# Kernel optimization log

Hardware: AMD Instinct MI355X
Metric: run time of the kernel (lower is better)

The kernel has to match this reference:

```python
import jax, jax.numpy as jnp
import numpy as np

B, S, E, H, P, F = 8, 512, 512, 8, 64, 2048
D = E // H  # head_dim = 64
EPS = 1e-5


def layernorm(x, g, b):
    mu = jnp.mean(x, axis=-1, keepdims=True)
    var = jnp.mean((x - mu) ** 2, axis=-1, keepdims=True)
    return (x - mu) * jax.lax.rsqrt(var + EPS) * g + b


def setup_inputs() -> dict:
    key = jax.random.key(0)
    ks = jax.random.split(key, 20)
    s = 1.0 / np.sqrt(E)
    inp = {
        "x": jax.random.normal(ks[0], (B, S, E), jnp.float32),
        "dist": jax.random.uniform(ks[1], (B, S, S), jnp.float32),
        "delatimes": jax.random.randint(ks[2], (B, S), 0, 128, jnp.int32),
        "mask": jnp.ones((B, S), jnp.int32),
        "wq_w": jax.random.uniform(ks[3], (E, E), jnp.float32, -s, s),
        "wq_b": jnp.zeros((E,), jnp.float32),
        "wk_w": jax.random.uniform(ks[4], (E, E), jnp.float32, -s, s),
        "wk_b": jnp.zeros((E,), jnp.float32),
        "wv_w": jax.random.uniform(ks[5], (E, E), jnp.float32, -s, s),
        "wv_b": jnp.zeros((E,), jnp.float32),
        "wo_w": jax.random.uniform(ks[6], (E, E), jnp.float32, -s, s),
        "wo_b": jnp.zeros((E,), jnp.float32),
        "pos_emb": jax.random.normal(ks[7], (2 * P + 1, D), jnp.float32),
        "w1": jax.random.uniform(ks[8], (E, F), jnp.float32, -s, s),
        "b1": jnp.zeros((F,), jnp.float32),
        "w2": jax.random.uniform(ks[9], (F, E), jnp.float32, -1.0 / np.sqrt(F), 1.0 / np.sqrt(F)),
        "b2": jnp.zeros((E,), jnp.float32),
        "ln1_g": jnp.ones((E,), jnp.float32),
        "ln1_b": jnp.zeros((E,), jnp.float32),
        "ln2_g": jnp.ones((E,), jnp.float32),
        "ln2_b": jnp.zeros((E,), jnp.float32),
    }
    return inp


def reference(x, dist, delatimes, mask, wq_w, wq_b, wk_w, wk_b, wv_w, wv_b,
              wo_w, wo_b, pos_emb, w1, b1, w2, b2, ln1_g, ln1_b, ln2_g, ln2_b):
    # relative-time embedding indices [B,S,S]
    rel = delatimes[:, None, :] - delatimes[:, :, None]
    idx = jnp.clip(rel, -P, P) + P
    z = pos_emb[idx]  # [B,S,S,D]

    def heads(t, w, b):
        return (t @ w + b).reshape(B, S, H, D).transpose(0, 2, 1, 3)  # [B,H,S,D]

    q = heads(x, wq_w, wq_b)
    k = heads(x, wk_w, wk_b)
    v = heads(x, wv_w, wv_b)

    scale = D ** -0.5
    scores = jnp.einsum('bhid,bhjd->bhij', q, k) + jnp.einsum('bhid,bijd->bhij', q, z)
    w = scores * scale + 0.6 * dist[:, None, :, :]
    pad = mask[:, None, None, :]  # [B,1,1,S]
    w = jnp.where(pad == 0, -1e9, w)
    aw = jax.nn.softmax(w, axis=-1)

    attn = jnp.einsum('bhij,bhjd->bhid', aw, v) + jnp.einsum('bhij,bijd->bhid', aw, z)
    concat = attn.transpose(0, 2, 1, 3).reshape(B, S, E)
    attn_out = layernorm(x + (concat @ wo_w + wo_b), ln1_g, ln1_b)

    ffn = jax.nn.relu(attn_out @ w1 + b1) @ w2 + b2
    return layernorm(attn_out + ffn, ln2_g, ln2_b)
```

## Files before the change

### kernel.cpp

```cpp
#include <hip/hip_runtime.h>
#include <hip/hip_bf16.h>

typedef __bf16 bf16x8 __attribute__((ext_vector_type(8)));
typedef float f32x4 __attribute__((ext_vector_type(4)));

#define TOKENS 4096
#define EDIM 512
#define FDIM 2048
#define SEQ 512
#define NHEAD 8
#define HDIM 64
#define QKVS 1536

__global__ __launch_bounds__(256) void prep(
    const float* __restrict__ wq_w, const float* __restrict__ wk_w,
    const float* __restrict__ wv_w, const float* __restrict__ wo_w,
    const float* __restrict__ w1, const float* __restrict__ w2,
    const float* __restrict__ x, const float* __restrict__ dist,
    const float* __restrict__ wq_b, const float* __restrict__ wk_b,
    const float* __restrict__ wv_b,
    __bf16* __restrict__ wqkvt, __bf16* __restrict__ wot,
    __bf16* __restrict__ w1t, __bf16* __restrict__ w2t,
    __bf16* __restrict__ xb, __bf16* __restrict__ distb,
    float* __restrict__ qkvb) {
  __shared__ float t[32][33];
  int bid = blockIdx.x;
  if (bid < 3072) {
    const float* src;
    __bf16* dst;
    int R = 512, C = 512, bx, by;
    if (bid < 1024) {
      int seg = bid >> 8, local = bid & 255;
      src = seg == 0 ? wq_w : seg == 1 ? wk_w : seg == 2 ? wv_w : wo_w;
      dst = seg == 0 ? wqkvt : seg == 1 ? wqkvt + 262144 : seg == 2 ? wqkvt + 524288 : wot;
      bx = local & 15; by = local >> 4;
    } else if (bid < 2048) {
      int local = bid - 1024; src = w1; dst = w1t; C = 2048;
      bx = local & 63; by = local >> 6;
    } else {
      int local = bid - 2048; src = w2; dst = w2t; R = 2048;
      bx = local & 15; by = local >> 4;
    }
    int c0 = bx * 32, r0 = by * 32;
    int tx = threadIdx.x & 31, ty = threadIdx.x >> 5;
    for (int rr = ty; rr < 32; rr += 8)
      t[rr][tx] = src[(size_t)(r0 + rr) * C + c0 + tx];
    __syncthreads();
    for (int rr = ty; rr < 32; rr += 8)
      dst[(size_t)(c0 + rr) * R + r0 + tx] = (__bf16)t[tx][rr];
  } else if (bid < 4096) {
    int i = (bid - 3072) * 256 + threadIdx.x;
    float4 a = ((const float4*)x)[i * 2];
    float4 b4 = ((const float4*)x)[i * 2 + 1];
    bf16x8 p;
    p[0] = (__bf16)a.x; p[1] = (__bf16)a.y; p[2] = (__bf16)a.z; p[3] = (__bf16)a.w;
    p[4] = (__bf16)b4.x; p[5] = (__bf16)b4.y; p[6] = (__bf16)b4.z; p[7] = (__bf16)b4.w;
    ((bf16x8*)xb)[i] = p;
  } else if (bid == 4096) {
    for (int i = threadIdx.x; i < 1536; i += 256)
      qkvb[i] = i < 512 ? wq_b[i] : i < 1024 ? wk_b[i - 512] : wv_b[i - 1024];
  } else {
    int i = (bid - 4097) * 256 + threadIdx.x;
    float4 a = ((const float4*)dist)[i * 2];
    float4 b4 = ((const float4*)dist)[i * 2 + 1];
    bf16x8 p;
    p[0] = (__bf16)a.x; p[1] = (__bf16)a.y; p[2] = (__bf16)a.z; p[3] = (__bf16)a.w;
    p[4] = (__bf16)b4.x; p[5] = (__bf16)b4.y; p[6] = (__bf16)b4.z; p[7] = (__bf16)b4.w;
    ((bf16x8*)distb)[i] = p;
  }
}

__device__ __forceinline__ void gl_lds16(const void* g, void* l) {
  __builtin_amdgcn_global_load_lds(
      (const __attribute__((address_space(1))) unsigned int*)(size_t)g,
      (__attribute__((address_space(3))) unsigned int*)(size_t)l, 16, 0, 0);
}

template <int BN>
__global__ __launch_bounds__(256) void gemm128(
    const __bf16* __restrict__ A, const __bf16* __restrict__ Bt,
    const float* __restrict__ bias, const float* __restrict__ resid,
    float* __restrict__ Cf, __bf16* __restrict__ Cb,
    int M, int N, int K, int relu) {
  constexpr int NI = BN / 32;
  __shared__ __attribute__((aligned(16))) __bf16 Asl[128 * 64];
  __shared__ __attribute__((aligned(16))) __bf16 Bsl[BN * 64];
  const int tid = threadIdx.x, w = tid >> 6, lane = tid & 63;
  const int c = lane & 15, g = lane >> 4;
  const int m0 = blockIdx.y * 128, n0 = blockIdx.x * BN;
  const int wr = w >> 1, wc = w & 1;
  f32x4 acc[4][NI] = {};
  const __bf16* Ab = A + (size_t)m0 * K;
  const __bf16* Bb = Bt + (size_t)n0 * K;

  for (int k0 = 0; k0 < K; k0 += 64) {
#pragma unroll
    for (int s = 0; s < 4; s++) {
      int L = (s * 256 + tid) * 16;
      int row = L >> 7;
      int lslot = ((L >> 4) & 7) ^ (row & 7);
      gl_lds16(Ab + (size_t)row * K + k0 + lslot * 8,
               (char*)Asl + s * 4096 + w * 1024);
    }
#pragma unroll
    for (int s = 0; s < NI; s++) {
      int L = (s * 256 + tid) * 16;
      int row = L >> 7;
      int lslot = ((L >> 4) & 7) ^ (row & 7);
      gl_lds16(Bb + (size_t)row * K + k0 + lslot * 8,
               (char*)Bsl + s * 4096 + w * 1024);
    }
    __syncthreads();

    bf16x8 af[4][2], bfr[NI][2];
#pragma unroll
    for (int mi = 0; mi < 4; mi++)
#pragma unroll
      for (int ko = 0; ko < 2; ko++) {
        int row = wr * 64 + mi * 16 + c;
        int ps = (ko * 4 + g) ^ (row & 7);
        af[mi][ko] = *(const bf16x8*)&Asl[row * 64 + ps * 8];
      }
#pragma unroll
    for (int ni = 0; ni < NI; ni++)
#pragma unroll
      for (int ko = 0; ko < 2; ko++) {
        int row = wc * (BN / 2) + ni * 16 + c;
        int ps = (ko * 4 + g) ^ (row & 7);
        bfr[ni][ko] = *(const bf16x8*)&Bsl[row * 64 + ps * 8];
      }
#pragma unroll
    for (int mi = 0; mi < 4; mi++)
#pragma unroll
      for (int ni = 0; ni < NI; ni++) {
        acc[mi][ni] = __builtin_amdgcn_mfma_f32_16x16x32_bf16(af[mi][0], bfr[ni][0], acc[mi][ni], 0, 0, 0);
        acc[mi][ni] = __builtin_amdgcn_mfma_f32_16x16x32_bf16(af[mi][1], bfr[ni][1], acc[mi][ni], 0, 0, 0);
      }
    __syncthreads();
  }

#pragma unroll
  for (int mi = 0; mi < 4; mi++)
#pragma unroll
    for (int ni = 0; ni < NI; ni++)
#pragma unroll
      for (int r = 0; r < 4; r++) {
        int row = m0 + wr * 64 + mi * 16 + g * 4 + r;
        int col = n0 + wc * (BN / 2) + ni * 16 + c;
        float v = acc[mi][ni][r] + bias[col];
        if (resid) v += resid[(size_t)row * N + col];
        if (relu) v = fmaxf(v, 0.f);
        if (Cf) Cf[(size_t)row * N + col] = v;
        if (Cb) Cb[(size_t)row * N + col] = (__bf16)v;
      }
}

__device__ inline void cvt16(const float* __restrict__ src, __bf16* dst) {
  float4 f0 = *(const float4*)(src);
  float4 f1 = *(const float4*)(src + 4);
  float4 f2 = *(const float4*)(src + 8);
  float4 f3 = *(const float4*)(src + 12);
  bf16x8 p0, p1;
  p0[0]=(__bf16)f0.x; p0[1]=(__bf16)f0.y; p0[2]=(__bf16)f0.z; p0[3]=(__bf16)f0.w;
  p0[4]=(__bf16)f1.x; p0[5]=(__bf16)f1.y; p0[6]=(__bf16)f1.z; p0[7]=(__bf16)f1.w;
  p1[0]=(__bf16)f2.x; p1[1]=(__bf16)f2.y; p1[2]=(__bf16)f2.z; p1[3]=(__bf16)f2.w;
  p1[4]=(__bf16)f3.x; p1[5]=(__bf16)f3.y; p1[6]=(__bf16)f3.z; p1[7]=(__bf16)f3.w;
  *(bf16x8*)(dst) = p0;
  *(bf16x8*)(dst + 8) = p1;
}

__global__ __launch_bounds__(256) void qz_shift(
    const __bf16* __restrict__ qb, const float* __restrict__ pos_emb,
    const int* __restrict__ dtimes, __bf16* __restrict__ QZg) {
  __shared__ __attribute__((aligned(16))) __bf16 peL[144][72];
  __shared__ __attribute__((aligned(16))) __bf16 QL[64][72];
  __shared__ __attribute__((aligned(16))) float qzf[64][144];
  const int tid = threadIdx.x, w = tid >> 6, l = tid & 63, c = l & 15, g = l >> 4;
  const int bid = blockIdx.x, qt = bid & 7, bh = bid >> 3, h = bh & 7, b = bh >> 3;
  const int qbase = qt * 64;
  const int r = tid >> 2, d0 = (tid & 3) * 16;

  for (int s = 0; s < 3; s++) {
    int rr = r + s * 64;
    if (rr >= 144) break;
    if (rr < 129) {
      cvt16(pos_emb + rr * 64 + d0, &peL[rr][d0]);
    } else {
      bf16x8 z = {};
      *(bf16x8*)&peL[rr][d0] = z;
      *(bf16x8*)&peL[rr][d0 + 8] = z;
    }
  }
  {
    const __bf16* qp = qb + ((size_t)(b * SEQ + qbase + r)) * QKVS + h * HDIM + d0;
    *(bf16x8*)&QL[r][d0] = *(const bf16x8*)qp;
    *(bf16x8*)&QL[r][d0 + 8] = *(const bf16x8*)(qp + 8);
  }
  __syncthreads();

  bf16x8 aq0 = *(bf16x8*)&QL[w * 16 + c][g * 8];
  bf16x8 aq1 = *(bf16x8*)&QL[w * 16 + c][32 + g * 8];
  for (int n = 0; n < 9; n++) {
    f32x4 acc = {};
    bf16x8 b0 = *(bf16x8*)&peL[n * 16 + c][g * 8];
    bf16x8 b1 = *(bf16x8*)&peL[n * 16 + c][32 + g * 8];
    acc = __builtin_amdgcn_mfma_f32_16x16x32_bf16(aq0, b0, acc, 0, 0, 0);
    acc = __builtin_amdgcn_mfma_f32_16x16x32_bf16(aq1, b1, acc, 0, 0, 0);
    int t = n * 16 + c;
    for (int r4 = 0; r4 < 4; r4++) qzf[w * 16 + g * 4 + r4][t] = acc[r4];
  }
  __syncthreads();

  int dti = dtimes[b * SEQ + qbase + r];
  int t0 = (tid & 3) * 32;
  for (int q4 = 0; q4 < 4; q4++) {
    bf16x8 o;
    for (int e = 0; e < 8; e++) {
      int tau = t0 + q4 * 8 + e;
      int t = min(max(tau - dti, -64), 64) + 64;
      o[e] = (__bf16)qzf[r][t];
    }
    *(bf16x8*)(QZg + ((size_t)(bh * SEQ + qbase + r)) * 128 + t0 + q4 * 8) = o;
  }
}

#define KL_OFF 18432
__global__ __launch_bounds__(256) void attn_fused(
    const __bf16* __restrict__ qb, const __bf16* __restrict__ kb,
    const __bf16* __restrict__ vb, const __bf16* __restrict__ distb,
    const int* __restrict__ dtimes, const int* __restrict__ maskp,
    const __bf16* __restrict__ QZg, const float* __restrict__ pos_emb,
    __bf16* __restrict__ outb) {
  __shared__ __attribute__((aligned(16))) char smem[75776];
  auto QL  = (__bf16(*)[72])(smem);
  auto PL  = (__bf16(*)[72])(smem + 9216);
  char* KLb = smem + KL_OFF;
  auto VT  = (__bf16(*)[72])(smem + 26624);
  auto B1h = (__bf16(*)[72])(smem + 35840);
  auto qzL = (__bf16(*)[136])(smem + 54272);
  int* dtsL = (int*)(smem + 71680);
  int* mskL = (int*)(smem + 73728);
  auto CLs = (float(*)[136])(smem);
  auto peT = (__bf16(*)[136])(smem + 34816);

  const int tid = threadIdx.x, w = tid >> 6, l = tid & 63, c = l & 15, g = l >> 4;
  const int bid = blockIdx.x;
  const int qt = bid & 7, h = (bid >> 3) & 7, b = bid >> 6, bh = bid >> 3;
  const int qbase = qt * 64;
  const int r = tid >> 2, d0 = (tid & 3) * 16;
  const int vd = l, vj0 = w * 16;

  auto stageK = [&](int jt) {
#pragma unroll
    for (int s = 0; s < 2; s++) {
      int L = (s * 256 + tid) * 16;
      int row = L >> 7;
      int sl = ((L >> 4) & 7) ^ (row & 7);
      gl_lds16(kb + ((size_t)(b * SEQ + jt * 64 + row)) * QKVS + h * HDIM + sl * 8,
               KLb + s * 4096 + w * 1024);
    }
  };
  __bf16 vreg[16];
  float dA[16], dB[16];
  auto loadV = [&](int jt) {
    const __bf16* vp = vb + ((size_t)(b * SEQ + jt * 64 + vj0)) * QKVS + h * HDIM + vd;
#pragma unroll
    for (int q = 0; q < 16; q++) vreg[q] = vp[(size_t)q * QKVS];
  };
  auto loadD = [&](int jt, float (&dd)[16]) {
#pragma unroll
    for (int n = 0; n < 4; n++)
#pragma unroll
      for (int r4 = 0; r4 < 4; r4++) {
        int il = w * 16 + g * 4 + r4;
        dd[n * 4 + r4] =
            (float)distb[((size_t)(b * SEQ + qbase + il)) * SEQ + jt * 64 + n * 16 + c];
      }
  };

  stageK(0); loadV(0); loadD(0, dA);

  {
    const __bf16* qp = qb + ((size_t)(b * SEQ + qbase + r)) * QKVS + h * HDIM + d0;
    *(bf16x8*)&QL[r][d0] = *(const bf16x8*)qp;
    *(bf16x8*)&QL[r][d0 + 8] = *(const bf16x8*)(qp + 8);
  }
  {
    int ch = (tid & 3) * 32;
    const __bf16* src = QZg + ((size_t)(bh * SEQ + qbase + r)) * 128 + ch;
    for (int q4 = 0; q4 < 4; q4++)
      *(bf16x8*)&qzL[r][ch + q4 * 8] = *(const bf16x8*)(src + q4 * 8);
  }
  for (int idx = tid; idx < SEQ; idx += 256) {
    dtsL[idx] = dtimes[b * SEQ + idx];
    mskL[idx] = maskp[b * SEQ + idx];
  }
  {
    bf16x8 z = {};
    for (int idx = tid; idx < 128 * 9; idx += 256)
      *(bf16x8*)&B1h[idx / 9][(idx % 9) * 8] = z;
  }
  __syncthreads();

  bf16x8 aq0 = *(bf16x8*)&QL[w * 16 + c][g * 8];
  bf16x8 aq1 = *(bf16x8*)&QL[w * 16 + c][32 + g * 8];
  float lsum[4] = {0.f, 0.f, 0.f, 0.f};
  f32x4 Oacc[4] = {};
  f32x4 Cacc[8] = {};

  auto body = [&](int jt, float (&dcur)[16], float (&dnxt)[16]) {
    __syncthreads();
    {
      bf16x8 pv0, pv1;
#pragma unroll
      for (int q = 0; q < 8; q++) { pv0[q] = vreg[q]; pv1[q] = vreg[q + 8]; }
      *(bf16x8*)&VT[vd][vj0] = pv0;
      *(bf16x8*)&VT[vd][vj0 + 8] = pv1;
    }
    if (tid < 64) {
      if (jt > 0) {
        int tp = dtsL[(jt - 1) * 64 + tid], tn = dtsL[jt * 64 + tid];
        if (tp != tn) B1h[tp][tid] = (__bf16)0.f;
        B1h[tn][tid] = (__bf16)1.f;
      } else {
        B1h[dtsL[tid]][tid] = (__bf16)1.f;
      }
    }
    if (jt < 7) { loadV(jt + 1); loadD(jt + 1, dnxt); }
    __syncthreads();

#pragma unroll
    for (int n = 0; n < 4; n++) {
      f32x4 acc = {};
      int row = n * 16 + c;
      bf16x8 bk0 = *(const bf16x8*)(KLb + row * 128 + ((g ^ (row & 7)) * 16));
      bf16x8 bk1 = *(const bf16x8*)(KLb + row * 128 + (((g + 4) ^ (row & 7)) * 16));
      acc = __builtin_amdgcn_mfma_f32_16x16x32_bf16(aq0, bk0, acc, 0, 0, 0);
      acc = __builtin_amdgcn_mfma_f32_16x16x32_bf16(aq1, bk1, acc, 0, 0, 0);
      int jl = n * 16 + c, jg = jt * 64 + jl;
      int dtj = dtsL[jg];
      int mk = mskL[jg];
#pragma unroll
      for (int r4 = 0; r4 < 4; r4++) {
        int il = w * 16 + g * 4 + r4;
        float s = (acc[r4] + (float)qzL[il][dtj]) * 0.125f + 0.6f * dcur[n * 4 + r4];
        float p = mk ? __expf(s) : 0.f;
        lsum[r4] += p;
        PL[il][jl] = (__bf16)p;
      }
    }
    __syncthreads();
    if (jt < 7) stageK(jt + 1);

    bf16x8 ap0 = *(bf16x8*)&PL[w * 16 + c][g * 8];
    bf16x8 ap1 = *(bf16x8*)&PL[w * 16 + c][32 + g * 8];
#pragma unroll
    for (int dn = 0; dn < 4; dn++) {
      bf16x8 bv0 = *(bf16x8*)&VT[dn * 16 + c][g * 8];
      bf16x8 bv1 = *(bf16x8*)&VT[dn * 16 + c][32 + g * 8];
      Oacc[dn] = __builtin_amdgcn_mfma_f32_16x16x32_bf16(ap0, bv0, Oacc[dn], 0, 0, 0);
      Oacc[dn] = __builtin_amdgcn_mfma_f32_16x16x32_bf16(ap1, bv1, Oacc[dn], 0, 0, 0);
    }
#pragma unroll
    for (int tn = 0; tn < 8; tn++) {
      bf16x8 bz0 = *(bf16x8*)&B1h[tn * 16 + c][g * 8];
      bf16x8 bz1 = *(bf16x8*)&B1h[tn * 16 + c][32 + g * 8];
      Cacc[tn] = __builtin_amdgcn_mfma_f32_16x16x32_bf16(ap0, bz0, Cacc[tn], 0, 0, 0);
      Cacc[tn] = __builtin_amdgcn_mfma_f32_16x16x32_bf16(ap1, bz1, Cacc[tn], 0, 0, 0);
    }
  };
  for (int jt2 = 0; jt2 < 8; jt2 += 2) {
    body(jt2, dA, dB);
    body(jt2 + 1, dB, dA);
  }

  __syncthreads();
  {
    float4 z4 = {0.f, 0.f, 0.f, 0.f};
    for (int idx = tid; idx < 64 * 34; idx += 256) ((float4*)CLs)[idx] = z4;
  }
  for (int s = 0; s < 3; s++) {
    int t = r + s * 64;
    if (t < 129) {
      float vals[16];
      *(float4*)&vals[0]  = *(const float4*)(pos_emb + t * 64 + d0);
      *(float4*)&vals[4]  = *(const float4*)(pos_emb + t * 64 + d0 + 4);
      *(float4*)&vals[8]  = *(const float4*)(pos_emb + t * 64 + d0 + 8);
      *(float4*)&vals[12] = *(const float4*)(pos_emb + t * 64 + d0 + 12);
#pragma unroll
      for (int q = 0; q < 16; q++) peT[d0 + q][t] = (__bf16)vals[q];
    }
  }
  __syncthreads();

  {
    int dti_r4[4];
#pragma unroll
    for (int r4 = 0; r4 < 4; r4++) dti_r4[r4] = dtsL[qbase + w * 16 + g * 4 + r4];
#pragma unroll
    for (int tn = 0; tn < 8; tn++)
#pragma unroll
      for (int r4 = 0; r4 < 4; r4++) {
        int il = w * 16 + g * 4 + r4;
        int tau = tn * 16 + c, d = tau - dti_r4[r4];
        float val = Cacc[tn][r4];
        if (d <= -64) atomicAdd(&CLs[il][0], val);
        else if (d >= 64) atomicAdd(&CLs[il][128], val);
        else CLs[il][d + 64] = val;
      }
  }
  __syncthreads();

  float linv[4];
#pragma unroll
  for (int r4 = 0; r4 < 4; r4++) {
    float s = lsum[r4];
    for (int off = 1; off < 16; off <<= 1) s += __shfl_xor(s, off);
    linv[r4] = 1.0f / s;
  }

  f32x4 acc2[4] = {};
#pragma unroll
  for (int ks = 0; ks < 4; ks++) {
    const float* ap = &CLs[w * 16 + c][ks * 32 + g * 8];
    float4 a0 = *(const float4*)ap, a1 = *(const float4*)(ap + 4);
    bf16x8 af;
    af[0]=(__bf16)a0.x; af[1]=(__bf16)a0.y; af[2]=(__bf16)a0.z; af[3]=(__bf16)a0.w;
    af[4]=(__bf16)a1.x; af[5]=(__bf16)a1.y; af[6]=(__bf16)a1.z; af[7]=(__bf16)a1.w;
#pragma unroll
    for (int dn = 0; dn < 4; dn++) {
      bf16x8 bf = *(bf16x8*)&peT[dn * 16 + c][ks * 32 + g * 8];
      acc2[dn] = __builtin_amdgcn_mfma_f32_16x16x32_bf16(af, bf, acc2[dn], 0, 0, 0);
    }
  }
#pragma unroll
  for (int r4 = 0; r4 < 4; r4++) {
    int il = w * 16 + g * 4 + r4;
    float c128 = CLs[il][128];
#pragma unroll
    for (int dn = 0; dn < 4; dn++) {
      int d = dn * 16 + c;
      float y = acc2[dn][r4] + c128 * (float)peT[d][128];
      outb[((size_t)(b * SEQ + qbase + il)) * EDIM + h * HDIM + d] =
          (__bf16)((Oacc[dn][r4] + y) * linv[r4]);
    }
  }
}

__global__ __launch_bounds__(256) void ln_kernel(
    const float* __restrict__ in, const float* __restrict__ g,
    const float* __restrict__ bta, float* __restrict__ out,
    __bf16* __restrict__ outb) {
  int row = blockIdx.x * 4 + (threadIdx.x >> 6), lane = threadIdx.x & 63;
  const float* p = in + (size_t)row * EDIM;
  float4 v0 = *(const float4*)(p + lane * 8);
  float4 v1 = *(const float4*)(p + lane * 8 + 4);
  float vals[8] = {v0.x, v0.y, v0.z, v0.w, v1.x, v1.y, v1.z, v1.w};
  float s = 0.f;
  for (int j = 0; j < 8; j++) s += vals[j];
  for (int o = 32; o; o >>= 1) s += __shfl_xor(s, o);
  float mu = s * (1.0f / EDIM);
  float vs = 0.f;
  for (int j = 0; j < 8; j++) {
    vals[j] -= mu;
    vs += vals[j] * vals[j];
  }
  for (int o = 32; o; o >>= 1) vs += __shfl_xor(vs, o);
  float rs = rsqrtf(vs * (1.0f / EDIM) + 1e-5f);
  for (int j = 0; j < 8; j++) {
    int col = lane * 8 + j;
    float v = vals[j] * rs * g[col] + bta[col];
    out[(size_t)row * EDIM + col] = v;
    if (outb) outb[(size_t)row * EDIM + col] = (__bf16)v;
  }
}

extern "C" void kernel_launch(void* const* d_in, const int* in_sizes, int n_in,
                              void* d_out, int out_size, void* d_ws, size_t ws_size,
                              hipStream_t stream) {
  const float* x = (const float*)d_in[0];
  const float* dist = (const float*)d_in[1];
  const int* dtimes = (const int*)d_in[2];
  const int* maskp = (const int*)d_in[3];
  const float* wq_w = (const float*)d_in[4];
  const float* wq_b = (const float*)d_in[5];
  const float* wk_w = (const float*)d_in[6];
  const float* wk_b = (const float*)d_in[7];
  const float* wv_w = (const float*)d_in[8];
  const float* wv_b = (const float*)d_in[9];
  const float* wo_w = (const float*)d_in[10];
  const float* wo_b = (const float*)d_in[11];
  const float* pos_emb = (const float*)d_in[12];
  const float* w1 = (const float*)d_in[13];
  const float* b1 = (const float*)d_in[14];
  const float* w2 = (const float*)d_in[15];
  const float* b2 = (const float*)d_in[16];
  const float* ln1_g = (const float*)d_in[17];
  const float* ln1_b = (const float*)d_in[18];
  const float* ln2_g = (const float*)d_in[19];
  const float* ln2_b = (const float*)d_in[20];
  float* out = (float*)d_out;

  const int M = TOKENS;
  const size_t T = TOKENS;
  float* fws = (float*)d_ws;

  __bf16* qkvB   = (__bf16*)fws;
  float*  ln2in  = fws;
  float*  wo_out = fws + T * 768;
  float*  attno  = fws + T * 1280;
  __bf16* QZg    = (__bf16*)(fws + T * 1792);
  __bf16* attnob = (__bf16*)(fws + T * 2304);
  __bf16* hid    = (__bf16*)(fws + T * 2560);
  __bf16* attnb  = (__bf16*)(fws + T * 3584);
  __bf16* xb     = (__bf16*)(fws + T * 3840);
  __bf16* wqkvt  = (__bf16*)(fws + T * 4096);
  __bf16* wot    = wqkvt + 1536 * 512;
  __bf16* w1t    = wot + 512 * 512;
  __bf16* w2t    = w1t + 512 * 2048;
  __bf16* distb  = w2t + 2048 * 512;
  float*  qkvb   = (float*)(distb + 2097152);

  prep<<<5121, 256, 0, stream>>>(wq_w, wk_w, wv_w, wo_w, w1, w2, x, dist,
                                 wq_b, wk_b, wv_b,
                                 wqkvt, wot, w1t, w2t, xb, distb, qkvb);

  gemm128<128><<<dim3(1536 / 128, M / 128), 256, 0, stream>>>(
      xb, wqkvt, qkvb, nullptr, nullptr, qkvB, M, 1536, 512, 0);

  qz_shift<<<512, 256, 0, stream>>>(qkvB, pos_emb, dtimes, QZg);
  attn_fused<<<512, 256, 0, stream>>>(qkvB, qkvB + 512, qkvB + 1024, distb,
                                      dtimes, maskp, QZg, pos_emb, attnb);

  gemm128<64><<<dim3(512 / 64, M / 128), 256, 0, stream>>>(
      attnb, wot, wo_b, x, wo_out, nullptr, M, 512, 512, 0);
  ln_kernel<<<M / 4, 256, 0, stream>>>(wo_out, ln1_g, ln1_b, attno, attnob);

  gemm128<128><<<dim3(2048 / 128, M / 128), 256, 0, stream>>>(
      attnob, w1t, b1, nullptr, nullptr, hid, M, 2048, 512, 1);
  gemm128<64><<<dim3(512 / 64, M / 128), 256, 0, stream>>>(
      hid, w2t, b2, attno, ln2in, nullptr, M, 512, 2048, 0);
  ln_kernel<<<M / 4, 256, 0, stream>>>(ln2in, ln2_g, ln2_b, out, nullptr);
}
```

Before: 286.1 us.

## Halve GEMM M-tile, add workgroup swizzle, and read LN1 residual as bf16

Makes the GEMM M-tile a template parameter and switches all four GEMMs from 128 to 64 rows, doubling the number of workgroups so more CUs have work on the small grids. It also remaps block IDs with a stride-8 swizzle to change which tiles run at the same time, aiming for better cache locality. The FFN2 residual now reads the bf16 LN1 output instead of a separate fp32 copy, so LN1 no longer writes fp32. The trade-offs are less reuse per tile, a slight precision loss in the residual, and a swizzle that assumes the workgroup count is divisible by 8.

```diff
diff --git a/kernel.cpp b/kernel.cpp
--- a/kernel.cpp
+++ b/kernel.cpp
@@ -76,26 +76,30 @@
       (__attribute__((address_space(3))) unsigned int*)(size_t)l, 16, 0, 0);
 }
 
-template <int BN>
+template <int BM, int BN>
 __global__ __launch_bounds__(256) void gemm128(
     const __bf16* __restrict__ A, const __bf16* __restrict__ Bt,
     const float* __restrict__ bias, const float* __restrict__ resid,
+    const __bf16* __restrict__ residb,
     float* __restrict__ Cf, __bf16* __restrict__ Cb,
     int M, int N, int K, int relu) {
-  constexpr int NI = BN / 32;
-  __shared__ __attribute__((aligned(16))) __bf16 Asl[128 * 64];
+  constexpr int MI = BM / 32, NI = BN / 32;
+  __shared__ __attribute__((aligned(16))) __bf16 Asl[BM * 64];
   __shared__ __attribute__((aligned(16))) __bf16 Bsl[BN * 64];
   const int tid = threadIdx.x, w = tid >> 6, lane = tid & 63;
   const int c = lane & 15, g = lane >> 4;
-  const int m0 = blockIdx.y * 128, n0 = blockIdx.x * BN;
+  const int nwg = gridDim.x * gridDim.y;
+  const int orig = blockIdx.y * gridDim.x + blockIdx.x;
+  const int swz = (orig & 7) * (nwg >> 3) + (orig >> 3);
+  const int m0 = (swz / gridDim.x) * BM, n0 = (swz % gridDim.x) * BN;
   const int wr = w >> 1, wc = w & 1;
-  f32x4 acc[4][NI] = {};
+  f32x4 acc[MI][NI] = {};
   const __bf16* Ab = A + (size_t)m0 * K;
   const __bf16* Bb = Bt + (size_t)n0 * K;
 
   for (int k0 = 0; k0 < K; k0 += 64) {
 #pragma unroll
-    for (int s = 0; s < 4; s++) {
+    for (int s = 0; s < BM / 32; s++) {
       int L = (s * 256 + tid) * 16;
       int row = L >> 7;
       int lslot = ((L >> 4) & 7) ^ (row & 7);
@@ -103,7 +107,7 @@
                (char*)Asl + s * 4096 + w * 1024);
     }
 #pragma unroll
-    for (int s = 0; s < NI; s++) {
+    for (int s = 0; s < BN / 32; s++) {
       int L = (s * 256 + tid) * 16;
       int row = L >> 7;
       int lslot = ((L >> 4) & 7) ^ (row & 7);
@@ -112,12 +116,12 @@
     }
     __syncthreads();
 
-    bf16x8 af[4][2], bfr[NI][2];
-#pragma unroll
-    for (int mi = 0; mi < 4; mi++)
+    bf16x8 af[MI][2], bfr[NI][2];
+#pragma unroll
+    for (int mi = 0; mi < MI; mi++)
 #pragma unroll
       for (int ko = 0; ko < 2; ko++) {
-        int row = wr * 64 + mi * 16 + c;
+        int row = wr * (BM / 2) + mi * 16 + c;
         int ps = (ko * 4 + g) ^ (row & 7);
         af[mi][ko] = *(const bf16x8*)&Asl[row * 64 + ps * 8];
       }
@@ -130,7 +134,7 @@
         bfr[ni][ko] = *(const bf16x8*)&Bsl[row * 64 + ps * 8];
       }
 #pragma unroll
-    for (int mi = 0; mi < 4; mi++)
+    for (int mi = 0; mi < MI; mi++)
 #pragma unroll
       for (int ni = 0; ni < NI; ni++) {
         acc[mi][ni] = __builtin_amdgcn_mfma_f32_16x16x32_bf16(af[mi][0], bfr[ni][0], acc[mi][ni], 0, 0, 0);
@@ -140,15 +144,16 @@
   }
 
 #pragma unroll
-  for (int mi = 0; mi < 4; mi++)
+  for (int mi = 0; mi < MI; mi++)
 #pragma unroll
     for (int ni = 0; ni < NI; ni++)
 #pragma unroll
       for (int r = 0; r < 4; r++) {
-        int row = m0 + wr * 64 + mi * 16 + g * 4 + r;
+        int row = m0 + wr * (BM / 2) + mi * 16 + g * 4 + r;
         int col = n0 + wc * (BN / 2) + ni * 16 + c;
         float v = acc[mi][ni][r] + bias[col];
         if (resid) v += resid[(size_t)row * N + col];
+        if (residb) v += (float)residb[(size_t)row * N + col];
         if (relu) v = fmaxf(v, 0.f);
         if (Cf) Cf[(size_t)row * N + col] = v;
         if (Cb) Cb[(size_t)row * N + col] = (__bf16)v;
@@ -470,7 +475,7 @@
   for (int j = 0; j < 8; j++) {
     int col = lane * 8 + j;
     float v = vals[j] * rs * g[col] + bta[col];
-    out[(size_t)row * EDIM + col] = v;
+    if (out) out[(size_t)row * EDIM + col] = v;
     if (outb) outb[(size_t)row * EDIM + col] = (__bf16)v;
   }
 }
@@ -508,7 +513,6 @@
   __bf16* qkvB   = (__bf16*)fws;
   float*  ln2in  = fws;
   float*  wo_out = fws + T * 768;
-  float*  attno  = fws + T * 1280;
   __bf16* QZg    = (__bf16*)(fws + T * 1792);
   __bf16* attnob = (__bf16*)(fws + T * 2304);
   __bf16* hid    = (__bf16*)(fws + T * 2560);
@@ -525,20 +529,20 @@
                                  wq_b, wk_b, wv_b,
                                  wqkvt, wot, w1t, w2t, xb, distb, qkvb);
 
-  gemm128<128><<<dim3(1536 / 128, M / 128), 256, 0, stream>>>(
-      xb, wqkvt, qkvb, nullptr, nullptr, qkvB, M, 1536, 512, 0);
+  gemm128<64, 128><<<dim3(1536 / 128, M / 64), 256, 0, stream>>>(
+      xb, wqkvt, qkvb, nullptr, nullptr, nullptr, qkvB, M, 1536, 512, 0);
 
   qz_shift<<<512, 256, 0, stream>>>(qkvB, pos_emb, dtimes, QZg);
   attn_fused<<<512, 256, 0, stream>>>(qkvB, qkvB + 512, qkvB + 1024, distb,
                                       dtimes, maskp, QZg, pos_emb, attnb);
 
-  gemm128<64><<<dim3(512 / 64, M / 128), 256, 0, stream>>>(
-      attnb, wot, wo_b, x, wo_out, nullptr, M, 512, 512, 0);
-  ln_kernel<<<M / 4, 256, 0, stream>>>(wo_out, ln1_g, ln1_b, attno, attnob);
-
-  gemm128<128><<<dim3(2048 / 128, M / 128), 256, 0, stream>>>(
-      attnob, w1t, b1, nullptr, nullptr, hid, M, 2048, 512, 1);
-  gemm128<64><<<dim3(512 / 64, M / 128), 256, 0, stream>>>(
-      hid, w2t, b2, attno, ln2in, nullptr, M, 512, 2048, 0);
+  gemm128<64, 64><<<dim3(512 / 64, M / 64), 256, 0, stream>>>(
+      attnb, wot, wo_b, x, nullptr, wo_out, nullptr, M, 512, 512, 0);
+  ln_kernel<<<M / 4, 256, 0, stream>>>(wo_out, ln1_g, ln1_b, nullptr, attnob);
+
+  gemm128<64, 128><<<dim3(2048 / 128, M / 64), 256, 0, stream>>>(
+      attnob, w1t, b1, nullptr, nullptr, nullptr, hid, M, 2048, 512, 1);
+  gemm128<64, 64><<<dim3(512 / 64, M / 64), 256, 0, stream>>>(
+      hid, w2t, b2, nullptr, attnob, ln2in, nullptr, M, 512, 2048, 0);
   ln_kernel<<<M / 4, 256, 0, stream>>>(ln2in, ln2_g, ln2_b, out, nullptr);
 }
```

Measured after the change: 249.7 us. 1.15x faster.
